# Kernel tuning notes

Hardware: AMD Instinct MI355X
Metric: run time of the kernel (lower is better)

The kernel has to match this reference:

```python
import jax, jax.numpy as jnp
import numpy as np

B, C, N, K, G = 4, 128, 4096, 9, 4


def setup_inputs() -> dict:
    key = jax.random.key(0)
    ks = jax.random.split(key, 4)
    s = 0.05
    return {
        "features": jax.random.normal(ks[0], (B, C, N, 1), jnp.float32),
        # Attn.linear: Conv2d(2C -> C, 1x1)
        "w_lin": jax.random.normal(ks[1], (C, 2 * C), jnp.float32) * s,
        "b_lin": jnp.zeros((C,), jnp.float32),
        # atten_weight_conv: Linear(C -> K*G)
        "w_aw": jax.random.normal(ks[2], (K * G, C), jnp.float32) * s,
        "b_aw": jnp.zeros((K * G,), jnp.float32),
        # GroupNorm(4, C)
        "gn_g": jnp.ones((C,), jnp.float32),
        "gn_b": jnp.zeros((C,), jnp.float32),
        # conv: Conv2d(C -> C, 1x1) + BatchNorm2d(C)
        "conv_w": jax.random.normal(ks[3], (C, C), jnp.float32) * s,
        "conv_b": jnp.zeros((C,), jnp.float32),
        "bn_g": jnp.ones((C,), jnp.float32),
        "bn_b": jnp.zeros((C,), jnp.float32),
    }


def reference(features, w_lin, b_lin, w_aw, b_aw, gn_g, gn_b, conv_w, conv_b, bn_g, bn_b):
    B, C, N, _ = features.shape
    K, G = 9, 4
    Cg = C // G  # 32 channels per group
    EPS = 1e-5

    x = features[..., 0]                       # [B,C,N]
    # ---- KNN graph (negative squared distance, top-k) ----
    xx = jnp.sum(x * x, axis=1)                # [B,N]
    inner = jnp.einsum('bcn,bcm->bnm', x, x)   # [B,N,N]
    pd = 2.0 * inner - xx[:, :, None] - xx[:, None, :]
    idx = jax.lax.top_k(pd, K)[1]              # [B,N,K]

    # ---- edge feature gather: cat(x, x - x_neighbor) ----
    xt = x.transpose(0, 2, 1)                  # [B,N,C]
    b_ix = jnp.arange(B)[:, None, None]
    nbr = xt[b_ix, idx]                        # [B,N,K,C]
    ctr = jnp.broadcast_to(xt[:, :, None, :], (B, N, K, C))
    edge = jnp.concatenate([ctr, ctr - nbr], axis=-1)   # [B,N,K,2C]

    # ---- Attn.linear (1x1 conv == per-position linear) ----
    feat = jnp.einsum('bnke,ce->bnkc', edge, w_lin) + b_lin  # [B,N,K,C]

    # ---- grouped channel attention (4 groups of 32) ----
    fg = feat.reshape(B, N, K, G, Cg)
    scores = jnp.einsum('bnkgc,bnjgc->bngkj', fg, fg) / np.sqrt(32.0)
    s = jax.nn.softmax(scores, axis=-1)        # [B,N,G,K,K]
    attn = jnp.einsum('bngkj,bnjgc->bngkc', s, jax.nn.elu(fg))  # [B,N,G,K,Cg]

    # ---- attention weights over neighbors ----
    aw = jnp.einsum('bnc,dc->bnd', xt, w_aw) + b_aw          # [B,N,K*G]
    aw = jax.nn.softmax(aw.reshape(B, N, G, K), axis=-1)     # [B,N,G,K]

    # ---- weighted neighbor combine ----
    lf = jnp.einsum('bngk,bngkc->bngc', aw, attn)            # [B,N,G,Cg]
    lf = lf.transpose(0, 2, 3, 1).reshape(B, C, N, 1)        # [B,C,N,1]

    # ---- GroupNorm(4, C) over residual ----
    y = lf + features
    yg = y.reshape(B, G, Cg * N)
    mu = yg.mean(-1, keepdims=True)
    var = yg.var(-1, keepdims=True)
    yn = ((yg - mu) / jnp.sqrt(var + EPS)).reshape(B, C, N, 1)
    yn = yn * gn_g[None, :, None, None] + gn_b[None, :, None, None]

    # ---- 1x1 conv + BatchNorm (training-mode batch stats) + ReLU ----
    z = jnp.einsum('oc,bcnk->bonk', conv_w, yn) + conv_b[None, :, None, None]
    m = z.mean(axis=(0, 2, 3), keepdims=True)
    v = z.var(axis=(0, 2, 3), keepdims=True)
    z = (z - m) / jnp.sqrt(v + EPS) * bn_g[None, :, None, None] + bn_b[None, :, None, None]
    return jax.nn.relu(z)
```

## Files before the change

### kernel.cpp

```cpp
#include <hip/hip_runtime.h>
#include <hip/hip_bf16.h>
#include <cstddef>

#define NPTS 4096
#define CCH  128
#define KNN  9
#define GRP  4
#define BB   4
#define OFF_XT    0u
#define OFF_XX    2097152u
#define OFF_XHI   2113536u
#define OFF_IDX   3162112u
#define OFF_O     3309568u
#define OFF_Y     8159232u
#define OFF_GNP   10256384u
#define OFF_GNA   10387456u
#define OFF_GND   10387968u
#define OFF_WP    10388480u
#define OFF_BIASP 10454016u
#define OFF_BNSUM 10454528u
#define OFF_BNSQ  10454656u
#define OFF_BNSC  10454784u
#define OFF_BNSH  10454912u

using bf16x8 = __attribute__((ext_vector_type(8))) short;
using f32x4  = __attribute__((ext_vector_type(4))) float;

typedef __attribute__((address_space(1))) const unsigned as1c_u32;
typedef __attribute__((address_space(3))) unsigned as3_u32;

#define CE(a, b) { float _h = fmaxf(a, b); b = fminf(a, b); a = _h; }

#define SENT_BITS 0xFF7FF000u

__global__ void k_transpose(const float* __restrict__ x, float* __restrict__ xt,
                            __hip_bfloat16* __restrict__ xhi, float* __restrict__ xx) {
  __shared__ float t[32][33];
  int tx = threadIdx.x, ty = threadIdx.y;
  int n0 = blockIdx.x * 32, c0 = blockIdx.y * 32, b = blockIdx.z;
  float v = x[((size_t)b * CCH + c0 + ty) * NPTS + n0 + tx];
  t[ty][tx] = v;
  __syncthreads();
  float tv = t[tx][ty];
  size_t R = (size_t)b * NPTS + n0 + ty;
  int c = c0 + tx;
  xt[R * CCH + c] = tv;
  int g = c >> 3, w = c & 7;
  int sc = (((g ^ ((n0 + ty) & 15)) << 3) | w);
  xhi[R * CCH + sc] = __float2bfloat16(tv);
  if (ty == 0) {
    float s = 0.f;
    #pragma unroll
    for (int k = 0; k < 32; k++) { float u = t[k][tx]; s += u * u; }
    atomicAdd(&xx[b * NPTS + n0 + tx], s);
  }
}

__launch_bounds__(256, 2)
__global__ void k_knn(const short* __restrict__ xhi, const float* __restrict__ xx,
                      float* __restrict__ cand) {
  __shared__ short Acs[2][16384];
  const int tid = threadIdx.x;
  const int wave = tid >> 6, lane = tid & 63;
  const int quad = lane >> 4, m = lane & 15;
  const int b = blockIdx.y;
  const int q0 = blockIdx.x * 32;
  const short* xb = xhi + (size_t)b * NPTS * CCH;
  const float* xxb = xx + (b << 12);

  const char* gsrc0 = (const char*)xb + wave * 8192 + lane * 16;

  #pragma unroll
  for (int i = 0; i < 8; i++)
    __builtin_amdgcn_global_load_lds((as1c_u32*)(gsrc0 + i * 1024),
                                     (as3_u32*)&Acs[0][wave * 4096 + i * 512],
                                     16, 0, 0);

  bf16x8 qfrag[2][4];
  #pragma unroll
  for (int qt = 0; qt < 2; qt++) {
    const short* qrow = xb + (size_t)(q0 + qt * 16 + m) * CCH;
    #pragma unroll
    for (int ks = 0; ks < 4; ks++) {
      int slot = (ks * 4 + quad) ^ m;
      qfrag[qt][ks] = *(const bf16x8*)(qrow + slot * 8);
    }
  }

  float top8[2][8];
  #pragma unroll
  for (int qt = 0; qt < 2; qt++)
    #pragma unroll
    for (int p = 0; p < 8; p++) top8[qt][p] = __uint_as_float(SENT_BITS);

  for (int c = 0; c < 32; c++) {
    __syncthreads();
    if (c < 31) {
      const char* gsrc = gsrc0 + (size_t)(c + 1) * 32768;
      int bi = (c + 1) & 1;
      #pragma unroll
      for (int i = 0; i < 8; i++)
        __builtin_amdgcn_global_load_lds((as1c_u32*)(gsrc + i * 1024),
                                         (as3_u32*)&Acs[bi][wave * 4096 + i * 512],
                                         16, 0, 0);
    }
    f32x4 cinit[2];
    #pragma unroll
    for (int ct = 0; ct < 2; ct++)
      #pragma unroll
      for (int r = 0; r < 4; r++)
        cinit[ct][r] = -0.5f * xxb[c * 128 + wave * 32 + ct * 16 + quad * 4 + r];

    const short* cur = &Acs[c & 1][0];
    f32x4 acc[2][2];
    #pragma unroll
    for (int ct = 0; ct < 2; ct++)
      #pragma unroll
      for (int qt = 0; qt < 2; qt++) acc[ct][qt] = cinit[ct];

    #pragma unroll
    for (int ks = 0; ks < 4; ks++) {
      bf16x8 af[2];
      #pragma unroll
      for (int ct = 0; ct < 2; ct++) {
        int row = wave * 32 + ct * 16 + m;
        int slot = (ks * 4 + quad) ^ m;
        af[ct] = *(const bf16x8*)&cur[row * 128 + slot * 8];
      }
      #pragma unroll
      for (int ct = 0; ct < 2; ct++)
        #pragma unroll
        for (int qt = 0; qt < 2; qt++)
          acc[ct][qt] = __builtin_amdgcn_mfma_f32_16x16x32_bf16(
              af[ct], qfrag[qt][ks], acc[ct][qt], 0, 0, 0);
    }

    const unsigned cbase = (unsigned)(c * 128 + wave * 32 + quad * 4);
    #pragma unroll
    for (int qt = 0; qt < 2; qt++) {
      float k[8];
      #pragma unroll
      for (int ct = 0; ct < 2; ct++)
        #pragma unroll
        for (int r = 0; r < 4; r++) {
          unsigned u = __float_as_uint(acc[ct][qt][r]);
          k[ct * 4 + r] = __uint_as_float((u & 0xFFFFF000u) |
                                          (cbase + (unsigned)(ct * 16 + r)));
        }
      CE(k[0],k[1]) CE(k[2],k[3]) CE(k[4],k[5]) CE(k[6],k[7])
      CE(k[0],k[2]) CE(k[1],k[3]) CE(k[4],k[6]) CE(k[5],k[7])
      CE(k[1],k[2]) CE(k[5],k[6])
      CE(k[0],k[4]) CE(k[1],k[5]) CE(k[2],k[6]) CE(k[3],k[7])
      CE(k[2],k[4]) CE(k[3],k[5])
      CE(k[1],k[2]) CE(k[3],k[4]) CE(k[5],k[6])
      float t[8];
      #pragma unroll
      for (int i = 0; i < 8; i++) t[i] = fmaxf(top8[qt][i], k[7 - i]);
      CE(t[0],t[4]) CE(t[1],t[5]) CE(t[2],t[6]) CE(t[3],t[7])
      CE(t[0],t[2]) CE(t[1],t[3]) CE(t[4],t[6]) CE(t[5],t[7])
      CE(t[0],t[1]) CE(t[2],t[3]) CE(t[4],t[5]) CE(t[6],t[7])
      #pragma unroll
      for (int i = 0; i < 8; i++) top8[qt][i] = t[i];
    }
  }

  int slot = wave * 4 + quad;
  #pragma unroll
  for (int qt = 0; qt < 2; qt++) {
    int q = q0 + qt * 16 + m;
    float* dst = cand + ((size_t)((b << 12) + q) * 16 + slot) * 8;
    #pragma unroll
    for (int p = 0; p < 8; p++) dst[p] = top8[qt][p];
  }
}

__launch_bounds__(256)
__global__ void k_rerank(const float* __restrict__ cand, const float* __restrict__ xt,
                         const float* __restrict__ xx, int* __restrict__ idxOut) {
  __shared__ __align__(16) float arr[4][128];
  __shared__ int selS[4][16];
  __shared__ float keyS[4][16];
  int tid = threadIdx.x, wave = tid >> 6, lane = tid & 63;
  int qg = blockIdx.x * 4 + wave;
  int b = qg >> 12;
  const float* src = cand + (size_t)qg * 128;
  float e1 = src[lane], e2 = src[lane + 64];
  arr[wave][lane] = e1; arr[wave][lane + 64] = e2;
  __syncthreads();
  int r1 = 0, r2 = 0;
  #pragma unroll 8
  for (int f = 0; f < 128; f += 4) {
    float4 fv = *(const float4*)&arr[wave][f];
    r1 += (fv.x > e1) + (fv.y > e1) + (fv.z > e1) + (fv.w > e1);
    r2 += (fv.x > e2) + (fv.y > e2) + (fv.z > e2) + (fv.w > e2);
  }
  if (r1 < 16) selS[wave][r1] = (int)(__float_as_uint(e1) & 0xFFFu);
  if (r2 < 16) selS[wave][r2] = (int)(__float_as_uint(e2) & 0xFFFu);
  __syncthreads();
  int cnum = lane >> 2, part = lane & 3;
  int cidx = selS[wave][cnum];
  const float* rq = xt + (size_t)qg * CCH;
  const float* rc = xt + ((size_t)(b << 12) + cidx) * CCH;
  float dot = 0.f;
  #pragma unroll
  for (int j = 0; j < 8; j++) {
    float4 a4 = *(const float4*)&rq[part * 32 + j * 4];
    float4 c4 = *(const float4*)&rc[part * 32 + j * 4];
    dot += a4.x * c4.x + a4.y * c4.y + a4.z * c4.z + a4.w * c4.w;
  }
  dot += __shfl_xor(dot, 1);
  dot += __shfl_xor(dot, 2);
  if (part == 0)
    keyS[wave][cnum] = fmaf(2.f, dot, -xx[(b << 12) + cidx]);
  __syncthreads();
  if (lane < 16) {
    float k = keyS[wave][lane]; int i = selS[wave][lane];
    int r = 0;
    #pragma unroll
    for (int f = 0; f < 16; f++) {
      float fk = keyS[wave][f]; int fi = selS[wave][f];
      r += (fk > k) || (fk == k && fi < i);
    }
    if (r < 9) idxOut[(size_t)qg * 9 + r] = i;
  }
}

__launch_bounds__(256)
__global__ void k_linear(const float* __restrict__ xt, const float* __restrict__ w_lin,
                         const float* __restrict__ b_lin, const float* __restrict__ w_aw,
                         const float* __restrict__ b_aw, float* __restrict__ O) {
  __shared__ __align__(16) float Xs[64 * 132];
  __shared__ __align__(16) float Ws[64 * 132];
  int tid = threadIdx.x;
  int tx = tid & 15, ty = tid >> 4;
  int p0 = blockIdx.x * 64, o0 = blockIdx.y * 64;
  #pragma unroll
  for (int i = 0; i < 8; i++) {
    int flat = tid + i * 256; int r = flat >> 5, c4 = flat & 31;
    *(float4*)&Xs[r * 132 + c4 * 4] = *(const float4*)&xt[(size_t)(p0 + r) * CCH + c4 * 4];
  }
  #pragma unroll
  for (int i = 0; i < 8; i++) {
    int flat = tid + i * 256; int r = flat >> 5, c4 = flat & 31;
    int o = o0 + r; float4 v;
    if (o < 128) {
      float4 a = *(const float4*)&w_lin[(size_t)o * 256 + c4 * 4];
      float4 c = *(const float4*)&w_lin[(size_t)o * 256 + 128 + c4 * 4];
      v = make_float4(a.x + c.x, a.y + c.y, a.z + c.z, a.w + c.w);
    } else if (o < 256) {
      v = *(const float4*)&w_lin[(size_t)(o - 128) * 256 + 128 + c4 * 4];
    } else if (o < 292) {
      v = *(const float4*)&w_aw[(size_t)(o - 256) * 128 + c4 * 4];
    } else v = make_float4(0.f, 0.f, 0.f, 0.f);
    *(float4*)&Ws[r * 132 + c4 * 4] = v;
  }
  __syncthreads();
  float acc[4][4] = {};
  #pragma unroll 2
  for (int kq = 0; kq < 32; kq++) {
    float4 xa[4], wb[4];
    #pragma unroll
    for (int i = 0; i < 4; i++) xa[i] = *(const float4*)&Xs[(ty * 4 + i) * 132 + kq * 4];
    #pragma unroll
    for (int j = 0; j < 4; j++) wb[j] = *(const float4*)&Ws[(tx + 16 * j) * 132 + kq * 4];
    #pragma unroll
    for (int i = 0; i < 4; i++)
      #pragma unroll
      for (int j = 0; j < 4; j++)
        acc[i][j] += xa[i].x * wb[j].x + xa[i].y * wb[j].y + xa[i].z * wb[j].z + xa[i].w * wb[j].w;
  }
  #pragma unroll
  for (int j = 0; j < 4; j++) {
    int o = o0 + tx + 16 * j;
    if (o < 292) {
      float bias = (o < 128) ? b_lin[o] : ((o < 256) ? 0.f : b_aw[o - 256]);
      #pragma unroll
      for (int i = 0; i < 4; i++)
        O[(size_t)(p0 + ty * 4 + i) * 296 + o] = acc[i][j] + bias;
    }
  }
}

__launch_bounds__(256)
__global__ void k_attn(const float* __restrict__ O, const int* __restrict__ idxArr,
                       const float* __restrict__ xt, float* __restrict__ Y,
                       float* __restrict__ gnPart) {
  __shared__ __align__(16) float fF[4][1188];
  __shared__ __align__(16) float scS[4][432];
  __shared__ float awS[4][48];
  __shared__ float w9S[4][48];
  __shared__ int tI[45], tJ[45];
  int tid = threadIdx.x;
  int wave = tid >> 6, l = tid & 63;
  int pos = blockIdx.x * 4 + wave;
  int b = pos >> 12;
  if (tid == 0) {
    int p = 0;
    for (int i = 0; i < 9; i++) for (int j = i; j < 9; j++) { tI[p] = i; tJ[p] = j; p++; }
  }
  int nbr[9];
  const float* Op = O + (size_t)pos * 296;
  #pragma unroll
  for (int k = 0; k < 9; k++) nbr[k] = idxArr[(size_t)pos * 9 + k];
  float2 u = *(const float2*)(Op + 2 * l);
  float* fFw = fF[wave];
  #pragma unroll
  for (int k = 0; k < 9; k++) {
    const float* vp = O + (size_t)((b << 12) + nbr[k]) * 296 + 128;
    float2 vv = *(const float2*)(vp + 2 * l);
    *(float2*)&fFw[k * 132 + 2 * l] = make_float2(u.x - vv.x, u.y - vv.y);
  }
  __syncthreads();
  #pragma unroll
  for (int r = 0; r < 3; r++) {
    int p = r * 64 + l;
    if (p < 180) {
      int g = p / 45, q = p - g * 45;
      int i = tI[q], j = tJ[q];
      const float* fi = fFw + i * 132 + g * 32;
      const float* fj = fFw + j * 132 + g * 32;
      float s = 0.f;
      #pragma unroll
      for (int t8 = 0; t8 < 8; t8++) {
        float4 a4 = *(const float4*)(fi + 4 * t8);
        float4 b4 = *(const float4*)(fj + 4 * t8);
        s += a4.x * b4.x + a4.y * b4.y + a4.z * b4.z + a4.w * b4.w;
      }
      s *= 0.17677669529663687f;
      scS[wave][(g * 9 + i) * 12 + j] = s;
      scS[wave][(g * 9 + j) * 12 + i] = s;
    }
  }
  __syncthreads();
  if (l < 36) {
    int g = l / 9, i = l - g * 9;
    float* rp = &scS[wave][(g * 9 + i) * 12];
    float mx = rp[0];
    #pragma unroll
    for (int j = 1; j < 9; j++) mx = fmaxf(mx, rp[j]);
    float e[9]; float sm = 0.f;
    #pragma unroll
    for (int j = 0; j < 9; j++) { e[j] = __expf(rp[j] - mx); sm += e[j]; }
    float inv = 1.f / sm;
    #pragma unroll
    for (int j = 0; j < 9; j++) rp[j] = e[j] * inv;
  } else if (l < 40) {
    int g = l - 36;
    float a[9]; float mx = -3.4e38f;
    #pragma unroll
    for (int k = 0; k < 9; k++) { a[k] = Op[256 + g * 9 + k]; mx = fmaxf(mx, a[k]); }
    float sm = 0.f;
    #pragma unroll
    for (int k = 0; k < 9; k++) { a[k] = __expf(a[k] - mx); sm += a[k]; }
    float inv = 1.f / sm;
    #pragma unroll
    for (int k = 0; k < 9; k++) awS[wave][g * 12 + k] = a[k] * inv;
  }
  __syncthreads();
  if (l < 36) {
    int g = l / 9, j = l - g * 9;
    float s = 0.f;
    #pragma unroll
    for (int i = 0; i < 9; i++) s += awS[wave][g * 12 + i] * scS[wave][(g * 9 + i) * 12 + j];
    w9S[wave][g * 12 + j] = s;
  }
  __syncthreads();
  int g = l >> 4;
  float w9r[9];
  #pragma unroll
  for (int j = 0; j < 9; j++) w9r[j] = w9S[wave][g * 12 + j];
  int c0 = 2 * l;
  float lf0 = 0.f, lf1 = 0.f;
  #pragma unroll
  for (int j = 0; j < 9; j++) {
    float2 f2 = *(const float2*)&fFw[j * 132 + c0];
    float e0 = f2.x > 0.f ? f2.x : __expf(f2.x) - 1.f;
    float e1 = f2.y > 0.f ? f2.y : __expf(f2.y) - 1.f;
    lf0 += w9r[j] * e0;
    lf1 += w9r[j] * e1;
  }
  float2 xv = *(const float2*)(xt + (size_t)pos * CCH + c0);
  float y0 = lf0 + xv.x, y1 = lf1 + xv.y;
  *(float2*)(Y + (size_t)pos * CCH + c0) = make_float2(y0, y1);
  float s1 = y0 + y1, s2 = y0 * y0 + y1 * y1;
  #pragma unroll
  for (int mm = 1; mm <= 8; mm <<= 1) { s1 += __shfl_xor(s1, mm); s2 += __shfl_xor(s2, mm); }
  if ((l & 15) == 0) {
    gnPart[(size_t)pos * 8 + g * 2]     = s1;
    gnPart[(size_t)pos * 8 + g * 2 + 1] = s2;
  }
}

__global__ void k_gnstats(const float* __restrict__ gnPart,
                          const float* __restrict__ gn_g, const float* __restrict__ gn_b,
                          float* __restrict__ gnA, float* __restrict__ gnD) {
  int bg = blockIdx.x; int b = bg >> 2, g = bg & 3;
  int tid = threadIdx.x;
  float s1 = 0.f, s2 = 0.f;
  for (int r = tid; r < NPTS; r += 256) {
    const float* p = gnPart + (size_t)(b * NPTS + r) * 8 + g * 2;
    s1 += p[0]; s2 += p[1];
  }
  __shared__ float r1[256], r2[256];
  r1[tid] = s1; r2[tid] = s2;
  __syncthreads();
  for (int off = 128; off > 0; off >>= 1) {
    if (tid < off) { r1[tid] += r1[tid + off]; r2[tid] += r2[tid + off]; }
    __syncthreads();
  }
  __shared__ float muS, rsS;
  if (tid == 0) {
    float mu = r1[0] * (1.f / 131072.f);
    float var = r2[0] * (1.f / 131072.f) - mu * mu;
    muS = mu; rsS = 1.f / sqrtf(var + 1e-5f);
  }
  __syncthreads();
  if (tid < 32) {
    int c = g * 32 + tid;
    float a = rsS * gn_g[c];
    gnA[b * 128 + c] = a;
    gnD[b * 128 + c] = gn_b[c] - muS * a;
  }
}

__global__ void k_fold(const float* __restrict__ conv_w, const float* __restrict__ conv_b,
                       const float* __restrict__ gnA, const float* __restrict__ gnD,
                       float* __restrict__ Wp, float* __restrict__ biasp) {
  int b = blockIdx.x; int tid = threadIdx.x;
  __shared__ float dS[128], aS[128];
  if (tid < 128) { dS[tid] = gnD[b * 128 + tid]; aS[tid] = gnA[b * 128 + tid]; }
  __syncthreads();
  for (int f = tid; f < 16384; f += 256)
    Wp[(size_t)b * 16384 + f] = conv_w[f] * aS[f & 127];
  if (tid < 128) {
    float s = conv_b[tid];
    for (int c = 0; c < 128; c++) s += conv_w[tid * 128 + c] * dS[c];
    biasp[b * 128 + tid] = s;
  }
}

__launch_bounds__(256)
__global__ void k_conv(const float* __restrict__ Y, const float* __restrict__ Wp,
                       const float* __restrict__ biasp, float* __restrict__ zpre,
                       float* __restrict__ bnSum, float* __restrict__ bnSq) {
  __shared__ __align__(16) float Ys[64 * 132];
  __shared__ __align__(16) float Ws[64 * 132];
  int tid = threadIdx.x;
  int tx = tid & 15, ty = tid >> 4;
  int n0 = blockIdx.x * 64, o0 = blockIdx.y * 64, b = blockIdx.z;
  #pragma unroll
  for (int i = 0; i < 8; i++) {
    int flat = tid + i * 256; int r = flat >> 5, c4 = flat & 31;
    *(float4*)&Ys[r * 132 + c4 * 4] = *(const float4*)&Y[(size_t)((b << 12) + n0 + r) * CCH + c4 * 4];
    *(float4*)&Ws[r * 132 + c4 * 4] = *(const float4*)&Wp[(size_t)b * 16384 + (size_t)(o0 + r) * 128 + c4 * 4];
  }
  __syncthreads();
  float acc[4][4] = {};
  #pragma unroll 2
  for (int kq = 0; kq < 32; kq++) {
    float4 wa[4], yb[4];
    #pragma unroll
    for (int i = 0; i < 4; i++) wa[i] = *(const float4*)&Ws[(ty * 4 + i) * 132 + kq * 4];
    #pragma unroll
    for (int j = 0; j < 4; j++) yb[j] = *(const float4*)&Ys[(tx + 16 * j) * 132 + kq * 4];
    #pragma unroll
    for (int i = 0; i < 4; i++)
      #pragma unroll
      for (int j = 0; j < 4; j++)
        acc[i][j] += wa[i].x * yb[j].x + wa[i].y * yb[j].y + wa[i].z * yb[j].z + wa[i].w * yb[j].w;
  }
  #pragma unroll
  for (int i = 0; i < 4; i++) {
    int o = o0 + ty * 4 + i;
    float bias = biasp[b * 128 + o];
    float p1 = 0.f, p2 = 0.f;
    #pragma unroll
    for (int j = 0; j < 4; j++) {
      float z = acc[i][j] + bias;
      zpre[(((size_t)((b << 7) + o)) << 12) + n0 + tx + 16 * j] = z;
      p1 += z; p2 += z * z;
    }
    #pragma unroll
    for (int mm = 1; mm <= 8; mm <<= 1) { p1 += __shfl_xor(p1, mm); p2 += __shfl_xor(p2, mm); }
    if (tx == 0) { atomicAdd(&bnSum[o], p1); atomicAdd(&bnSq[o], p2); }
  }
}

__global__ void k_bnfin(const float* __restrict__ bnSum, const float* __restrict__ bnSq,
                        const float* __restrict__ bn_g, const float* __restrict__ bn_b,
                        float* __restrict__ bnScale, float* __restrict__ bnShift) {
  int o = threadIdx.x;
  float m = bnSum[o] * (1.f / 16384.f);
  float v = bnSq[o] * (1.f / 16384.f) - m * m;
  float sc = bn_g[o] / sqrtf(v + 1e-5f);
  bnScale[o] = sc;
  bnShift[o] = bn_b[o] - m * sc;
}

__global__ void k_final(const float* __restrict__ zpre, const float* __restrict__ bnScale,
                        const float* __restrict__ bnShift, float* __restrict__ out) {
  int i4 = blockIdx.x * 256 + threadIdx.x;
  int e = i4 * 4;
  int o = (e >> 12) & 127;
  float4 z = *(const float4*)&zpre[e];
  float sc = bnScale[o], sh = bnShift[o];
  float4 r;
  r.x = fmaxf(fmaf(z.x, sc, sh), 0.f);
  r.y = fmaxf(fmaf(z.y, sc, sh), 0.f);
  r.z = fmaxf(fmaf(z.z, sc, sh), 0.f);
  r.w = fmaxf(fmaf(z.w, sc, sh), 0.f);
  *(float4*)&out[e] = r;
}

extern "C" void kernel_launch(void* const* d_in, const int* in_sizes, int n_in,
                              void* d_out, int out_size, void* d_ws, size_t ws_size,
                              hipStream_t stream) {
  const float* features = (const float*)d_in[0];
  const float* w_lin  = (const float*)d_in[1];
  const float* b_lin  = (const float*)d_in[2];
  const float* w_aw   = (const float*)d_in[3];
  const float* b_aw   = (const float*)d_in[4];
  const float* gn_g   = (const float*)d_in[5];
  const float* gn_b   = (const float*)d_in[6];
  const float* conv_w = (const float*)d_in[7];
  const float* conv_b = (const float*)d_in[8];
  const float* bn_g   = (const float*)d_in[9];
  const float* bn_b   = (const float*)d_in[10];

  float* ws    = (float*)d_ws;
  float* xt    = ws + OFF_XT;
  float* xxp   = ws + OFF_XX;
  __hip_bfloat16* xhip = (__hip_bfloat16*)(ws + OFF_XHI);
  int*   idxp  = (int*)(ws + OFF_IDX);
  float* Op    = ws + OFF_O;
  float* candp = ws + OFF_O;
  float* Yp    = ws + OFF_Y;
  float* gnp   = ws + OFF_GNP;
  float* gnA   = ws + OFF_GNA;
  float* gnD   = ws + OFF_GND;
  float* Wp    = ws + OFF_WP;
  float* biasp = ws + OFF_BIASP;
  float* bnSum = ws + OFF_BNSUM;
  float* bnSq  = ws + OFF_BNSQ;
  float* bnSc  = ws + OFF_BNSC;
  float* bnSh  = ws + OFF_BNSH;
  float* zpre  = xt;

  hipMemsetAsync(xxp, 0, NPTS * BB * sizeof(float), stream);
  hipMemsetAsync(bnSum, 0, 256 * sizeof(float), stream);

  k_transpose<<<dim3(128, 4, 4), dim3(32, 32), 0, stream>>>(features, xt, xhip, xxp);
  k_knn<<<dim3(128, 4), 256, 0, stream>>>((const short*)xhip, xxp, candp);
  k_rerank<<<4096, 256, 0, stream>>>(candp, xt, xxp, idxp);
  k_linear<<<dim3(256, 5), 256, 0, stream>>>(xt, w_lin, b_lin, w_aw, b_aw, Op);
  k_attn<<<4096, 256, 0, stream>>>(Op, idxp, xt, Yp, gnp);
  k_gnstats<<<16, 256, 0, stream>>>(gnp, gn_g, gn_b, gnA, gnD);
  k_fold<<<4, 256, 0, stream>>>(conv_w, conv_b, gnA, gnD, Wp, biasp);
  k_conv<<<dim3(64, 2, 4), 256, 0, stream>>>(Yp, Wp, biasp, zpre, bnSum, bnSq);
  k_bnfin<<<1, 128, 0, stream>>>(bnSum, bnSq, bn_g, bn_b, bnSc, bnSh);
  k_final<<<2048, 256, 0, stream>>>(zpre, bnSc, bnSh, (float*)d_out);
}
```

Measured before the change: 275.6 us.

## Load KNN candidate tiles directly to registers and overlap selection with MFMA

The KNN kernel no longer stages candidate tiles in LDS through double-buffered global_load_lds with per-chunk barriers. Each wave now reads its bf16 fragments straight from global memory into registers. The top-8 selection network for the previous chunk runs while the current chunk's loads are in flight, making it a software pipeline. Launch bounds are raised to 3 blocks per SM. This removes the LDS use and block-wide syncs, but each wave must issue its own global loads, relying on L2 cache hits, and register pressure goes up.

```diff
diff --git a/kernel.cpp b/kernel.cpp
--- a/kernel.cpp
+++ b/kernel.cpp
@@ -26,9 +26,6 @@
 using bf16x8 = __attribute__((ext_vector_type(8))) short;
 using f32x4  = __attribute__((ext_vector_type(4))) float;
 
-typedef __attribute__((address_space(1))) const unsigned as1c_u32;
-typedef __attribute__((address_space(3))) unsigned as3_u32;
-
 #define CE(a, b) { float _h = fmaxf(a, b); b = fminf(a, b); a = _h; }
 
 #define SENT_BITS 0xFF7FF000u
@@ -56,10 +53,41 @@
   }
 }
 
-__launch_bounds__(256, 2)
+__device__ __forceinline__ void select_chunk(int c, int wave, int quad,
+                                             const f32x4 (&acc)[2][2],
+                                             float (&top8)[2][8]) {
+  const unsigned cbase = (unsigned)(c * 128 + wave * 32 + quad * 4);
+  #pragma unroll
+  for (int qt = 0; qt < 2; qt++) {
+    float k[8];
+    #pragma unroll
+    for (int ct = 0; ct < 2; ct++)
+      #pragma unroll
+      for (int r = 0; r < 4; r++) {
+        unsigned u = __float_as_uint(acc[ct][qt][r]);
+        k[ct * 4 + r] = __uint_as_float((u & 0xFFFFF000u) |
+                                        (cbase + (unsigned)(ct * 16 + r)));
+      }
+    CE(k[0],k[1]) CE(k[2],k[3]) CE(k[4],k[5]) CE(k[6],k[7])
+    CE(k[0],k[2]) CE(k[1],k[3]) CE(k[4],k[6]) CE(k[5],k[7])
+    CE(k[1],k[2]) CE(k[5],k[6])
+    CE(k[0],k[4]) CE(k[1],k[5]) CE(k[2],k[6]) CE(k[3],k[7])
+    CE(k[2],k[4]) CE(k[3],k[5])
+    CE(k[1],k[2]) CE(k[3],k[4]) CE(k[5],k[6])
+    float t[8];
+    #pragma unroll
+    for (int i = 0; i < 8; i++) t[i] = fmaxf(top8[qt][i], k[7 - i]);
+    CE(t[0],t[4]) CE(t[1],t[5]) CE(t[2],t[6]) CE(t[3],t[7])
+    CE(t[0],t[2]) CE(t[1],t[3]) CE(t[4],t[6]) CE(t[5],t[7])
+    CE(t[0],t[1]) CE(t[2],t[3]) CE(t[4],t[5]) CE(t[6],t[7])
+    #pragma unroll
+    for (int i = 0; i < 8; i++) top8[qt][i] = t[i];
+  }
+}
+
+__launch_bounds__(256, 3)
 __global__ void k_knn(const short* __restrict__ xhi, const float* __restrict__ xx,
                       float* __restrict__ cand) {
-  __shared__ short Acs[2][16384];
   const int tid = threadIdx.x;
   const int wave = tid >> 6, lane = tid & 63;
   const int quad = lane >> 4, m = lane & 15;
@@ -68,14 +96,6 @@
   const short* xb = xhi + (size_t)b * NPTS * CCH;
   const float* xxb = xx + (b << 12);
 
-  const char* gsrc0 = (const char*)xb + wave * 8192 + lane * 16;
-
-  #pragma unroll
-  for (int i = 0; i < 8; i++)
-    __builtin_amdgcn_global_load_lds((as1c_u32*)(gsrc0 + i * 1024),
-                                     (as3_u32*)&Acs[0][wave * 4096 + i * 512],
-                                     16, 0, 0);
-
   bf16x8 qfrag[2][4];
   #pragma unroll
   for (int qt = 0; qt < 2; qt++) {
@@ -87,82 +107,50 @@
     }
   }
 
+  int aoff[2][4];
+  #pragma unroll
+  for (int ct = 0; ct < 2; ct++)
+    #pragma unroll
+    for (int ks = 0; ks < 4; ks++)
+      aoff[ct][ks] = (wave * 32 + ct * 16 + m) * CCH + (((ks * 4 + quad) ^ m) * 8);
+
   float top8[2][8];
   #pragma unroll
   for (int qt = 0; qt < 2; qt++)
     #pragma unroll
     for (int p = 0; p < 8; p++) top8[qt][p] = __uint_as_float(SENT_BITS);
 
+  f32x4 acc[2][2];
+
   for (int c = 0; c < 32; c++) {
-    __syncthreads();
-    if (c < 31) {
-      const char* gsrc = gsrc0 + (size_t)(c + 1) * 32768;
-      int bi = (c + 1) & 1;
-      #pragma unroll
-      for (int i = 0; i < 8; i++)
-        __builtin_amdgcn_global_load_lds((as1c_u32*)(gsrc + i * 1024),
-                                         (as3_u32*)&Acs[bi][wave * 4096 + i * 512],
-                                         16, 0, 0);
-    }
+    bf16x8 af[2][4];
+    const short* cb = xb + c * (128 * CCH);
+    #pragma unroll
+    for (int ct = 0; ct < 2; ct++)
+      #pragma unroll
+      for (int ks = 0; ks < 4; ks++)
+        af[ct][ks] = *(const bf16x8*)(cb + aoff[ct][ks]);
     f32x4 cinit[2];
     #pragma unroll
     for (int ct = 0; ct < 2; ct++)
       #pragma unroll
       for (int r = 0; r < 4; r++)
         cinit[ct][r] = -0.5f * xxb[c * 128 + wave * 32 + ct * 16 + quad * 4 + r];
-
-    const short* cur = &Acs[c & 1][0];
-    f32x4 acc[2][2];
+    if (c > 0) select_chunk(c - 1, wave, quad, acc, top8);
     #pragma unroll
     for (int ct = 0; ct < 2; ct++)
       #pragma unroll
       for (int qt = 0; qt < 2; qt++) acc[ct][qt] = cinit[ct];
-
-    #pragma unroll
-    for (int ks = 0; ks < 4; ks++) {
-      bf16x8 af[2];
-      #pragma unroll
-      for (int ct = 0; ct < 2; ct++) {
-        int row = wave * 32 + ct * 16 + m;
-        int slot = (ks * 4 + quad) ^ m;
-        af[ct] = *(const bf16x8*)&cur[row * 128 + slot * 8];
-      }
+    #pragma unroll
+    for (int ks = 0; ks < 4; ks++)
       #pragma unroll
       for (int ct = 0; ct < 2; ct++)
         #pragma unroll
         for (int qt = 0; qt < 2; qt++)
           acc[ct][qt] = __builtin_amdgcn_mfma_f32_16x16x32_bf16(
-              af[ct], qfrag[qt][ks], acc[ct][qt], 0, 0, 0);
-    }
-
-    const unsigned cbase = (unsigned)(c * 128 + wave * 32 + quad * 4);
-    #pragma unroll
-    for (int qt = 0; qt < 2; qt++) {
-      float k[8];
-      #pragma unroll
-      for (int ct = 0; ct < 2; ct++)
-        #pragma unroll
-        for (int r = 0; r < 4; r++) {
-          unsigned u = __float_as_uint(acc[ct][qt][r]);
-          k[ct * 4 + r] = __uint_as_float((u & 0xFFFFF000u) |
-                                          (cbase + (unsigned)(ct * 16 + r)));
-        }
-      CE(k[0],k[1]) CE(k[2],k[3]) CE(k[4],k[5]) CE(k[6],k[7])
-      CE(k[0],k[2]) CE(k[1],k[3]) CE(k[4],k[6]) CE(k[5],k[7])
-      CE(k[1],k[2]) CE(k[5],k[6])
-      CE(k[0],k[4]) CE(k[1],k[5]) CE(k[2],k[6]) CE(k[3],k[7])
-      CE(k[2],k[4]) CE(k[3],k[5])
-      CE(k[1],k[2]) CE(k[3],k[4]) CE(k[5],k[6])
-      float t[8];
-      #pragma unroll
-      for (int i = 0; i < 8; i++) t[i] = fmaxf(top8[qt][i], k[7 - i]);
-      CE(t[0],t[4]) CE(t[1],t[5]) CE(t[2],t[6]) CE(t[3],t[7])
-      CE(t[0],t[2]) CE(t[1],t[3]) CE(t[4],t[6]) CE(t[5],t[7])
-      CE(t[0],t[1]) CE(t[2],t[3]) CE(t[4],t[5]) CE(t[6],t[7])
-      #pragma unroll
-      for (int i = 0; i < 8; i++) top8[qt][i] = t[i];
-    }
-  }
+              af[ct][ks], qfrag[qt][ks], acc[ct][qt], 0, 0, 0);
+  }
+  select_chunk(31, wave, quad, acc, top8);
 
   int slot = wave * 4 + quad;
   #pragma unroll
```

Result: slower. 295.6 us (+7.2%).
